# Optimization experiments

Hardware: AMD Instinct MI355X
Metric: run time of the kernel (lower is better)

Reference implementation:

```python
import jax, jax.numpy as jnp
import numpy as np
import math

C = 256
GROUPS = 8  # min(8, C)
EPS = 1e-5


def group_norm(x, gamma, beta):
    # x: [b, c, h, w]
    b, c, h, w = x.shape
    xg = x.reshape(b, GROUPS, c // GROUPS, h, w)
    mean = xg.mean(axis=(2, 3, 4), keepdims=True)
    var = xg.var(axis=(2, 3, 4), keepdims=True)
    xg = (xg - mean) / jnp.sqrt(var + EPS)
    x = xg.reshape(b, c, h, w)
    return x * gamma[None, :, None, None] + beta[None, :, None, None]


def setup_inputs() -> dict:
    key = jax.random.key(0)
    ks = jax.random.split(key, 7)
    b, h, w = 8, 64, 64
    x = jax.random.normal(ks[0], (b, C, h, w), dtype=jnp.float32)
    gn_w = jnp.ones((C,), dtype=jnp.float32)
    gn_b = jnp.zeros((C,), dtype=jnp.float32)
    # 1x1 convs as [out, in] matrices (kaiming-uniform-like scale)
    s = 1.0 / math.sqrt(C)
    qkv_w = jax.random.uniform(ks[1], (3 * C, C), minval=-s, maxval=s, dtype=jnp.float32)
    qkv_b = jax.random.uniform(ks[2], (3 * C,), minval=-s, maxval=s, dtype=jnp.float32)
    out_w = jax.random.uniform(ks[3], (C, C), minval=-s, maxval=s, dtype=jnp.float32)
    out_b = jax.random.uniform(ks[4], (C,), minval=-s, maxval=s, dtype=jnp.float32)
    return {"x": x, "gn_w": gn_w, "gn_b": gn_b, "qkv_w": qkv_w,
            "qkv_b": qkv_b, "out_w": out_w, "out_b": out_b}


def reference(x, gn_w, gn_b, qkv_w, qkv_b, out_w, out_b):
    b, c, h, w = x.shape
    xn = group_norm(x, gn_w, gn_b)  # residual uses normalized x (as in source)
    # 1x1 conv to qkv: [b, 3c, h, w]
    qkv = jnp.einsum('oc,bchw->bohw', qkv_w, xn) + qkv_b[None, :, None, None]
    q, k, v = jnp.split(qkv, 3, axis=1)
    # flatten spatial -> [b, hw, c]
    def flat(t):
        return t.transpose(0, 2, 3, 1).reshape(b, h * w, c)
    q, k, v = flat(q), flat(k), flat(v)
    scores = jnp.einsum('bnc,bmc->bnm', q, k) / math.sqrt(c)  # [b, hw, hw]
    attn = jax.nn.softmax(scores, axis=-1)
    out = jnp.einsum('bnm,bmc->bnc', attn, v)  # [b, hw, c]
    out = out.reshape(b, h, w, c).transpose(0, 3, 1, 2)  # [b, c, h, w]
    out = jnp.einsum('oc,bchw->bohw', out_w, out) + out_b[None, :, None, None]
    return out + xn
```

## Files before the change

kernel.cpp:

```cpp
#include <hip/hip_runtime.h>
#include <hip/hip_bf16.h>

#define BATCH 8
#define CH 256
#define HWSZ 4096
#define NGROUPS 8
#define CPG 32
#define GSIZE (CPG * HWSZ)

typedef unsigned short u16;
typedef short bf16x8 __attribute__((ext_vector_type(8)));
typedef float f32x4 __attribute__((ext_vector_type(4)));
typedef unsigned int u32x4 __attribute__((ext_vector_type(4)));

union Frag8 {
    bf16x8 v;
    u32x4 q;
    u16 s[8];
};

static __device__ inline u16 f2bf(float f) {
    unsigned int u = __float_as_uint(f);
    u = u + 0x7fffu + ((u >> 16) & 1u);
    return (u16)(u >> 16);
}

static __device__ inline unsigned int pk2bf(float a, float b) {
    __hip_bfloat162 h2 = __float22bfloat162_rn(make_float2(a, b));
    unsigned int r;
    __builtin_memcpy(&r, &h2, 4);
    return r;
}

__global__ __launch_bounds__(256) void gn_stats_part_k(const float* __restrict__ x,
                                                       float* __restrict__ partial) {
    int blk = blockIdx.x;
    int bg = blk >> 3, chunk = blk & 7;
    const float4* base = (const float4*)(x + (size_t)bg * GSIZE + (size_t)chunk * (GSIZE / 8));
    float s = 0.f, ss = 0.f;
    for (int i = threadIdx.x; i < GSIZE / 8 / 4; i += 256) {
        float4 v = base[i];
        s += v.x + v.y + v.z + v.w;
        ss += v.x * v.x + v.y * v.y + v.z * v.z + v.w * v.w;
    }
    #pragma unroll
    for (int off = 32; off > 0; off >>= 1) {
        s += __shfl_xor(s, off, 64);
        ss += __shfl_xor(ss, off, 64);
    }
    __shared__ float red[8];
    int wid = threadIdx.x >> 6;
    if ((threadIdx.x & 63) == 0) { red[wid * 2] = s; red[wid * 2 + 1] = ss; }
    __syncthreads();
    if (threadIdx.x == 0) {
        float S = red[0] + red[2] + red[4] + red[6];
        float SS = red[1] + red[3] + red[5] + red[7];
        atomicAdd(&partial[bg * 2], S);
        atomicAdd(&partial[bg * 2 + 1], SS);
    }
}

__global__ void gn_finalize_k(const float* __restrict__ partial, float* __restrict__ stats) {
    int bg = threadIdx.x;
    float S = partial[bg * 2], SS = partial[bg * 2 + 1];
    float mean = S / (float)GSIZE;
    float var = SS / (float)GSIZE - mean * mean;
    stats[bg * 2] = mean;
    stats[bg * 2 + 1] = rsqrtf(var + 1e-5f);
}

#define TPAD 258
__global__ __launch_bounds__(256) void gn_apply_k(const float* __restrict__ x,
                                                  const float* __restrict__ stats,
                                                  const float* __restrict__ gw,
                                                  const float* __restrict__ gb,
                                                  float* __restrict__ xnf,
                                                  u16* __restrict__ xnt) {
    int b = blockIdx.x >> 6;
    int hw0 = (blockIdx.x & 63) * 64;
    __shared__ u16 lds[64 * TPAD];
    __shared__ float sw[CH], sb[CH], smean[NGROUPS], srstd[NGROUPS];
    if (threadIdx.x < CH) { sw[threadIdx.x] = gw[threadIdx.x]; sb[threadIdx.x] = gb[threadIdx.x]; }
    if (threadIdx.x < NGROUPS) {
        smean[threadIdx.x] = stats[(b * NGROUPS + threadIdx.x) * 2];
        srstd[threadIdx.x] = stats[(b * NGROUPS + threadIdx.x) * 2 + 1];
    }
    __syncthreads();
    for (int it = 0; it < 64; ++it) {
        int idx = it * 256 + threadIdx.x;
        int c = idx >> 6, hwl = idx & 63;
        size_t g = ((size_t)b * CH + c) * HWSZ + hw0 + hwl;
        float v = x[g];
        int grp = c >> 5;
        float xn = (v - smean[grp]) * srstd[grp] * sw[c] + sb[c];
        xnf[g] = xn;
        lds[hwl * TPAD + c] = f2bf(xn);
    }
    __syncthreads();
    int hwl = threadIdx.x >> 2, cb = (threadIdx.x & 3) * 64;
    u16* dst = xnt + ((size_t)b * HWSZ + hw0 + hwl) * CH + cb;
    for (int j = 0; j < 64; j += 8) {
        u16 tmp[8];
        #pragma unroll
        for (int k = 0; k < 8; ++k) tmp[k] = lds[hwl * TPAD + cb + j + k];
        *(u32x4*)(dst + j) = *(u32x4*)tmp;
    }
}

__global__ __launch_bounds__(256) void qkv_gemm_k(const float* __restrict__ w,
                                                  const float* __restrict__ bias,
                                                  const u16* __restrict__ xnt,
                                                  u16* __restrict__ qws,
                                                  u16* __restrict__ kws,
                                                  u16* __restrict__ vws) {
    int b = blockIdx.z;
    int o0 = blockIdx.y * 64;
    int n0 = blockIdx.x * 64;
    int w_id = threadIdx.x >> 6;
    int lane = threadIdx.x & 63;
    int jr = lane & 15, g = lane >> 4;
    int orow = o0 + w_id * 16 + jr;
    f32x4 acc[4] = {};
    for (int kk = 0; kk < 8; ++kk) {
        const float* ap = w + (size_t)orow * CH + kk * 32 + g * 8;
        Frag8 af;
        #pragma unroll
        for (int e = 0; e < 8; ++e) af.s[e] = f2bf(ap[e]);
        #pragma unroll
        for (int s = 0; s < 4; ++s) {
            const u16* bp = xnt + ((size_t)b * HWSZ + n0 + s * 16 + jr) * CH + kk * 32 + g * 8;
            Frag8 bfr; bfr.q = *(const u32x4*)bp;
            acc[s] = __builtin_amdgcn_mfma_f32_16x16x32_bf16(af.v, bfr.v, acc[s], 0, 0, 0);
        }
    }
    #pragma unroll
    for (int s = 0; s < 4; ++s) {
        #pragma unroll
        for (int r = 0; r < 4; ++r) {
            int o = o0 + w_id * 16 + g * 4 + r;
            int n = n0 + s * 16 + jr;
            float val = acc[s][r] + bias[o];
            if (o < 256)       qws[((size_t)b * HWSZ + n) * CH + o] = f2bf(val * 0.0625f);
            else if (o < 512)  kws[((size_t)b * HWSZ + n) * CH + (o - 256)] = f2bf(val);
            else               vws[((size_t)b * CH + (o - 512)) * HWSZ + n] = f2bf(val);
        }
    }
}

#define PSTRIDE 72
#define NW 8
__global__ __launch_bounds__(512, 1) void attn_k(const u16* __restrict__ qws,
                                                 const u16* __restrict__ kws,
                                                 const u16* __restrict__ vws,
                                                 u16* __restrict__ ows) {
    __shared__ u16 kbuf[2][64 * 256];
    __shared__ u16 vbuf[2][256 * 64];
    __shared__ u16 plds[NW][16 * PSTRIDE];

    int b = blockIdx.y;
    int q0 = blockIdx.x * 128;
    int tid = threadIdx.x;
    int w_id = tid >> 6;
    int lane = tid & 63;
    int jr = lane & 15, g = lane >> 4;

    const char* kgbase = (const char*)(kws + ((size_t)b * HWSZ) * CH);
    const char* vgbase = (const char*)(vws + ((size_t)b * CH) * HWSZ);

    Frag8 qa[8];
    const u16* qbase = qws + ((size_t)b * HWSZ + q0 + w_id * 16 + jr) * CH;
    #pragma unroll
    for (int kk = 0; kk < 8; ++kk) qa[kk].q = *(const u32x4*)(qbase + kk * 32 + g * 8);

    auto stage = [&](int bufi, int kt) {
        int k0 = kt * 64;
        char* kd = (char*)&kbuf[bufi][0];
        char* vd = (char*)&vbuf[bufi][0];
        #pragma unroll
        for (int ii = 0; ii < 4; ++ii) {
            int i = w_id * 4 + ii;
            int r = i * 2 + (lane >> 5);
            int bl = (lane & 31) * 16;
            int bs = bl ^ ((r & 7) << 4);
            const char* src = kgbase + ((size_t)(k0 + r)) * 512 + bs;
            __builtin_amdgcn_global_load_lds(
                (const __attribute__((address_space(1))) void*)src,
                (__attribute__((address_space(3))) void*)(kd + i * 1024), 16, 0, 0);
        }
        #pragma unroll
        for (int ii = 0; ii < 4; ++ii) {
            int i = w_id * 4 + ii;
            int r = i * 8 + (lane >> 3);
            int bl = (lane & 7) * 16;
            int bs = bl ^ ((r & 7) << 4);
            const char* src = vgbase + (size_t)r * 8192 + (size_t)k0 * 2 + bs;
            __builtin_amdgcn_global_load_lds(
                (const __attribute__((address_space(1))) void*)src,
                (__attribute__((address_space(3))) void*)(vd + i * 1024), 16, 0, 0);
        }
    };

    float m_run = -1e30f, l_run = 0.f;
    f32x4 acc[16] = {};

    stage(0, 0);
    int bufi = 0;

    for (int kt = 0; kt < 64; ++kt) {
        if (kt + 1 < 64) {
            stage(bufi ^ 1, kt + 1);
            asm volatile("s_waitcnt vmcnt(8)" ::: "memory");
        } else {
            asm volatile("s_waitcnt vmcnt(0)" ::: "memory");
        }
        __builtin_amdgcn_s_barrier();

        const char* kb = (const char*)&kbuf[bufi][0];
        const char* vb = (const char*)&vbuf[bufi][0];

        f32x4 sacc[4] = {};
        __builtin_amdgcn_s_setprio(1);
        #pragma unroll
        for (int kk = 0; kk < 8; ++kk) {
            #pragma unroll
            for (int s = 0; s < 4; ++s) {
                int r = s * 16 + jr;
                int cb = kk * 64 + g * 16;
                Frag8 kf; kf.q = *(const u32x4*)(kb + r * 512 + (cb ^ ((r & 7) << 4)));
                sacc[s] = __builtin_amdgcn_mfma_f32_16x16x32_bf16(kf.v, qa[kk].v, sacc[s], 0, 0, 0);
            }
        }
        __builtin_amdgcn_s_setprio(0);

        float mx = sacc[0][0];
        #pragma unroll
        for (int s = 0; s < 4; ++s)
            #pragma unroll
            for (int r = 0; r < 4; ++r) mx = fmaxf(mx, sacc[s][r]);
        mx = fmaxf(mx, __shfl_xor(mx, 16, 64));
        mx = fmaxf(mx, __shfl_xor(mx, 32, 64));

        if (__any(mx > m_run + 8.f)) {
            float mnew = fmaxf(m_run, mx);
            float alpha = __expf(m_run - mnew);
            #pragma unroll
            for (int cs = 0; cs < 16; ++cs)
                #pragma unroll
                for (int r = 0; r < 4; ++r) acc[cs][r] *= alpha;
            l_run *= alpha;
            m_run = mnew;
        }

        float p[4][4];
        float rs = 0.f;
        #pragma unroll
        for (int s = 0; s < 4; ++s)
            #pragma unroll
            for (int r = 0; r < 4; ++r) {
                float pv = __expf(sacc[s][r] - m_run);
                p[s][r] = pv;
                rs += pv;
            }
        rs += __shfl_xor(rs, 16, 64);
        rs += __shfl_xor(rs, 32, 64);
        l_run += rs;

        #pragma unroll
        for (int s = 0; s < 4; ++s)
            #pragma unroll
            for (int i = 0; i < 2; ++i) {
                unsigned int pk = pk2bf(p[s][2 * i], p[s][2 * i + 1]);
                *(unsigned int*)&plds[w_id][jr * PSTRIDE + s * 16 + g * 4 + 2 * i] = pk;
            }

        __builtin_amdgcn_s_setprio(1);
        #pragma unroll
        for (int kk = 0; kk < 2; ++kk) {
            Frag8 pa;
            pa.q = *(const u32x4*)&plds[w_id][jr * PSTRIDE + kk * 32 + g * 8];
            #pragma unroll
            for (int cs = 0; cs < 16; ++cs) {
                int r = cs * 16 + jr;
                int cb = kk * 64 + g * 16;
                Frag8 vf; vf.q = *(const u32x4*)(vb + r * 128 + (cb ^ ((r & 7) << 4)));
                acc[cs] = __builtin_amdgcn_mfma_f32_16x16x32_bf16(vf.v, pa.v, acc[cs], 0, 0, 0);
            }
        }
        __builtin_amdgcn_s_setprio(0);

        asm volatile("s_waitcnt lgkmcnt(0)" ::: "memory");
        __builtin_amdgcn_s_barrier();
        bufi ^= 1;
    }

    float inv_l = 1.0f / l_run;
    int n = q0 + w_id * 16 + jr;
    u16* obase = ows + ((size_t)b * HWSZ + n) * CH;
    #pragma unroll
    for (int cs = 0; cs < 16; ++cs) {
        #pragma unroll
        for (int i = 0; i < 2; ++i) {
            int c = cs * 16 + g * 4 + 2 * i;
            unsigned int pk = pk2bf(acc[cs][2 * i] * inv_l, acc[cs][2 * i + 1] * inv_l);
            *(unsigned int*)&obase[c] = pk;
        }
    }
}

__global__ __launch_bounds__(256) void proj_k(const float* __restrict__ w,
                                              const float* __restrict__ bias,
                                              const u16* __restrict__ ows,
                                              const float* __restrict__ xnf,
                                              float* __restrict__ out) {
    int b = blockIdx.z;
    int o0 = blockIdx.y * 64;
    int n0 = blockIdx.x * 64;
    int w_id = threadIdx.x >> 6;
    int lane = threadIdx.x & 63;
    int jr = lane & 15, g = lane >> 4;
    int orow = o0 + w_id * 16 + jr;
    f32x4 acc[4] = {};
    for (int kk = 0; kk < 8; ++kk) {
        const float* ap = w + (size_t)orow * CH + kk * 32 + g * 8;
        Frag8 af;
        #pragma unroll
        for (int e = 0; e < 8; ++e) af.s[e] = f2bf(ap[e]);
        #pragma unroll
        for (int s = 0; s < 4; ++s) {
            const u16* bp = ows + ((size_t)b * HWSZ + n0 + s * 16 + jr) * CH + kk * 32 + g * 8;
            Frag8 bfr; bfr.q = *(const u32x4*)bp;
            acc[s] = __builtin_amdgcn_mfma_f32_16x16x32_bf16(af.v, bfr.v, acc[s], 0, 0, 0);
        }
    }
    #pragma unroll
    for (int s = 0; s < 4; ++s) {
        #pragma unroll
        for (int r = 0; r < 4; ++r) {
            int o = o0 + w_id * 16 + g * 4 + r;
            int n = n0 + s * 16 + jr;
            size_t gaddr = ((size_t)b * CH + o) * HWSZ + n;
            out[gaddr] = acc[s][r] + bias[o] + xnf[gaddr];
        }
    }
}

extern "C" void kernel_launch(void* const* d_in, const int* in_sizes, int n_in,
                              void* d_out, int out_size, void* d_ws, size_t ws_size,
                              hipStream_t stream) {
    const float* x     = (const float*)d_in[0];
    const float* gn_w  = (const float*)d_in[1];
    const float* gn_b  = (const float*)d_in[2];
    const float* qkv_w = (const float*)d_in[3];
    const float* qkv_b = (const float*)d_in[4];
    const float* out_w = (const float*)d_in[5];
    const float* out_b = (const float*)d_in[6];
    float* out = (float*)d_out;

    char* ws = (char*)d_ws;
    const size_t NB = (size_t)BATCH * HWSZ * CH;
    float* stats   = (float*)ws;
    float* partial = (float*)(ws + 512);
    float* xnf     = (float*)(ws + 1024);
    size_t off = 1024 + NB * 4;
    u16* xnt = (u16*)(ws + off); off += NB * 2;
    u16* qws = (u16*)(ws + off); off += NB * 2;
    u16* kws = (u16*)(ws + off); off += NB * 2;
    u16* vws = (u16*)(ws + off); off += NB * 2;
    u16* ows = (u16*)(ws + off); off += NB * 2;

    hipMemsetAsync(partial, 0, 64 * 2 * sizeof(float), stream);
    gn_stats_part_k<<<dim3(512), dim3(256), 0, stream>>>(x, partial);
    gn_finalize_k<<<dim3(1), dim3(64), 0, stream>>>(partial, stats);
    gn_apply_k<<<dim3(512), dim3(256), 0, stream>>>(x, stats, gn_w, gn_b, xnf, xnt);
    qkv_gemm_k<<<dim3(64, 12, 8), dim3(256), 0, stream>>>(qkv_w, qkv_b, xnt, qws, kws, vws);
    attn_k<<<dim3(32, 8), dim3(512), 0, stream>>>(qws, kws, vws, ows);
    proj_k<<<dim3(64, 4, 8), dim3(256), 0, stream>>>(out_w, out_b, ows, xnf, out);
}
```

Measured before the change: 484.3 us.

## Switch attention to 32x32x16 MFMA with register-resident P and 4 waves

The attention kernel moves from 16x16x32 MFMA tiles to 32x32x16 tiles, with each wave owning 32 query rows and the block shrinking from 8 to 4 waves. The P matrix is now rearranged into B-operand fragments with cross-half lane shuffles instead of a round trip through LDS, so the per-wave P buffer is removed. Larger tiles raise the compute per LDS fragment load of K and V. The cost is higher register pressure from 128 accumulator floats and fewer waves to hide latency, and each wave now issues twice as many staging loads.

```diff
diff --git a/kernel.cpp b/kernel.cpp
--- a/kernel.cpp
+++ b/kernel.cpp
@@ -9,8 +9,10 @@
 #define GSIZE (CPG * HWSZ)
 
 typedef unsigned short u16;
+typedef unsigned int u32;
 typedef short bf16x8 __attribute__((ext_vector_type(8)));
 typedef float f32x4 __attribute__((ext_vector_type(4)));
+typedef float f32x16 __attribute__((ext_vector_type(16)));
 typedef unsigned int u32x4 __attribute__((ext_vector_type(4)));
 
 union Frag8 {
@@ -25,9 +27,9 @@
     return (u16)(u >> 16);
 }
 
-static __device__ inline unsigned int pk2bf(float a, float b) {
+static __device__ inline u32 pk2bf(float a, float b) {
     __hip_bfloat162 h2 = __float22bfloat162_rn(make_float2(a, b));
-    unsigned int r;
+    u32 r;
     __builtin_memcpy(&r, &h2, 4);
     return r;
 }
@@ -147,38 +149,36 @@
     }
 }
 
-#define PSTRIDE 72
-#define NW 8
-__global__ __launch_bounds__(512, 1) void attn_k(const u16* __restrict__ qws,
+__global__ __launch_bounds__(256, 1) void attn_k(const u16* __restrict__ qws,
                                                  const u16* __restrict__ kws,
                                                  const u16* __restrict__ vws,
                                                  u16* __restrict__ ows) {
     __shared__ u16 kbuf[2][64 * 256];
     __shared__ u16 vbuf[2][256 * 64];
-    __shared__ u16 plds[NW][16 * PSTRIDE];
 
     int b = blockIdx.y;
     int q0 = blockIdx.x * 128;
     int tid = threadIdx.x;
     int w_id = tid >> 6;
     int lane = tid & 63;
-    int jr = lane & 15, g = lane >> 4;
+    int qcol = lane & 31;
+    int hi = lane >> 5;
 
     const char* kgbase = (const char*)(kws + ((size_t)b * HWSZ) * CH);
     const char* vgbase = (const char*)(vws + ((size_t)b * CH) * HWSZ);
 
-    Frag8 qa[8];
-    const u16* qbase = qws + ((size_t)b * HWSZ + q0 + w_id * 16 + jr) * CH;
-    #pragma unroll
-    for (int kk = 0; kk < 8; ++kk) qa[kk].q = *(const u32x4*)(qbase + kk * 32 + g * 8);
+    Frag8 qf[16];
+    const u16* qbase = qws + ((size_t)b * HWSZ + q0 + w_id * 32 + qcol) * CH + hi * 8;
+    #pragma unroll
+    for (int ks = 0; ks < 16; ++ks) qf[ks].q = *(const u32x4*)(qbase + ks * 16);
 
     auto stage = [&](int bufi, int kt) {
         int k0 = kt * 64;
         char* kd = (char*)&kbuf[bufi][0];
         char* vd = (char*)&vbuf[bufi][0];
         #pragma unroll
-        for (int ii = 0; ii < 4; ++ii) {
-            int i = w_id * 4 + ii;
+        for (int ii = 0; ii < 8; ++ii) {
+            int i = w_id * 8 + ii;
             int r = i * 2 + (lane >> 5);
             int bl = (lane & 31) * 16;
             int bs = bl ^ ((r & 7) << 4);
@@ -188,8 +188,8 @@
                 (__attribute__((address_space(3))) void*)(kd + i * 1024), 16, 0, 0);
         }
         #pragma unroll
-        for (int ii = 0; ii < 4; ++ii) {
-            int i = w_id * 4 + ii;
+        for (int ii = 0; ii < 8; ++ii) {
+            int i = w_id * 8 + ii;
             int r = i * 8 + (lane >> 3);
             int bl = (lane & 7) * 16;
             int bs = bl ^ ((r & 7) << 4);
@@ -201,7 +201,7 @@
     };
 
     float m_run = -1e30f, l_run = 0.f;
-    f32x4 acc[16] = {};
+    f32x16 acc[8] = {};
 
     stage(0, 0);
     int bufi = 0;
@@ -209,7 +209,7 @@
     for (int kt = 0; kt < 64; ++kt) {
         if (kt + 1 < 64) {
             stage(bufi ^ 1, kt + 1);
-            asm volatile("s_waitcnt vmcnt(8)" ::: "memory");
+            asm volatile("s_waitcnt vmcnt(16)" ::: "memory");
         } else {
             asm volatile("s_waitcnt vmcnt(0)" ::: "memory");
         }
@@ -218,72 +218,89 @@
         const char* kb = (const char*)&kbuf[bufi][0];
         const char* vb = (const char*)&vbuf[bufi][0];
 
-        f32x4 sacc[4] = {};
+        f32x16 sacc[2] = {};
         __builtin_amdgcn_s_setprio(1);
         #pragma unroll
-        for (int kk = 0; kk < 8; ++kk) {
-            #pragma unroll
-            for (int s = 0; s < 4; ++s) {
-                int r = s * 16 + jr;
-                int cb = kk * 64 + g * 16;
+        for (int ks = 0; ks < 16; ++ks) {
+            #pragma unroll
+            for (int t = 0; t < 2; ++t) {
+                int r = t * 32 + qcol;
+                int cb = ks * 32 + hi * 16;
                 Frag8 kf; kf.q = *(const u32x4*)(kb + r * 512 + (cb ^ ((r & 7) << 4)));
-                sacc[s] = __builtin_amdgcn_mfma_f32_16x16x32_bf16(kf.v, qa[kk].v, sacc[s], 0, 0, 0);
+                sacc[t] = __builtin_amdgcn_mfma_f32_32x32x16_bf16(kf.v, qf[ks].v, sacc[t], 0, 0, 0);
             }
         }
         __builtin_amdgcn_s_setprio(0);
 
         float mx = sacc[0][0];
         #pragma unroll
-        for (int s = 0; s < 4; ++s)
-            #pragma unroll
-            for (int r = 0; r < 4; ++r) mx = fmaxf(mx, sacc[s][r]);
-        mx = fmaxf(mx, __shfl_xor(mx, 16, 64));
+        for (int t = 0; t < 2; ++t)
+            #pragma unroll
+            for (int e = 0; e < 16; ++e) mx = fmaxf(mx, sacc[t][e]);
         mx = fmaxf(mx, __shfl_xor(mx, 32, 64));
 
         if (__any(mx > m_run + 8.f)) {
             float mnew = fmaxf(m_run, mx);
             float alpha = __expf(m_run - mnew);
             #pragma unroll
-            for (int cs = 0; cs < 16; ++cs)
+            for (int dt = 0; dt < 8; ++dt)
                 #pragma unroll
-                for (int r = 0; r < 4; ++r) acc[cs][r] *= alpha;
+                for (int e = 0; e < 16; ++e) acc[dt][e] *= alpha;
             l_run *= alpha;
             m_run = mnew;
         }
 
-        float p[4][4];
+        float p_[2][16];
         float rs = 0.f;
         #pragma unroll
-        for (int s = 0; s < 4; ++s)
-            #pragma unroll
-            for (int r = 0; r < 4; ++r) {
-                float pv = __expf(sacc[s][r] - m_run);
-                p[s][r] = pv;
+        for (int t = 0; t < 2; ++t)
+            #pragma unroll
+            for (int e = 0; e < 16; ++e) {
+                float pv = __expf(sacc[t][e] - m_run);
+                p_[t][e] = pv;
                 rs += pv;
             }
-        rs += __shfl_xor(rs, 16, 64);
         rs += __shfl_xor(rs, 32, 64);
         l_run += rs;
 
-        #pragma unroll
-        for (int s = 0; s < 4; ++s)
-            #pragma unroll
-            for (int i = 0; i < 2; ++i) {
-                unsigned int pk = pk2bf(p[s][2 * i], p[s][2 * i + 1]);
-                *(unsigned int*)&plds[w_id][jr * PSTRIDE + s * 16 + g * 4 + 2 * i] = pk;
+        u32 pk_[2][4][2];
+        #pragma unroll
+        for (int t = 0; t < 2; ++t)
+            #pragma unroll
+            for (int d = 0; d < 4; ++d) {
+                pk_[t][d][0] = pk2bf(p_[t][4 * d + 0], p_[t][4 * d + 1]);
+                pk_[t][d][1] = pk2bf(p_[t][4 * d + 2], p_[t][4 * d + 3]);
             }
 
+        Frag8 pf[4];
+        #pragma unroll
+        for (int kstep = 0; kstep < 4; ++kstep) {
+            const int j0 = 2 * kstep, j1 = 2 * kstep + 1;
+            u32 x0a = pk_[j0 >> 2][j0 & 3][0], x0b = pk_[j0 >> 2][j0 & 3][1];
+            u32 x1a = pk_[j1 >> 2][j1 & 3][0], x1b = pk_[j1 >> 2][j1 & 3][1];
+            u32 s0 = hi ? x0a : x1a;
+            u32 s1 = hi ? x0b : x1b;
+            u32 r0 = __shfl_xor(s0, 32, 64);
+            u32 r1 = __shfl_xor(s1, 32, 64);
+            u32 a0 = hi ? x1a : x0a;
+            u32 a1 = hi ? x1b : x0b;
+            u32x4 f;
+            f[0] = hi ? r0 : a0;
+            f[1] = hi ? r1 : a1;
+            f[2] = hi ? a0 : r0;
+            f[3] = hi ? a1 : r1;
+            pf[kstep].q = f;
+        }
+
         __builtin_amdgcn_s_setprio(1);
         #pragma unroll
-        for (int kk = 0; kk < 2; ++kk) {
-            Frag8 pa;
-            pa.q = *(const u32x4*)&plds[w_id][jr * PSTRIDE + kk * 32 + g * 8];
-            #pragma unroll
-            for (int cs = 0; cs < 16; ++cs) {
-                int r = cs * 16 + jr;
-                int cb = kk * 64 + g * 16;
-                Frag8 vf; vf.q = *(const u32x4*)(vb + r * 128 + (cb ^ ((r & 7) << 4)));
-                acc[cs] = __builtin_amdgcn_mfma_f32_16x16x32_bf16(vf.v, pa.v, acc[cs], 0, 0, 0);
+        for (int dt = 0; dt < 8; ++dt) {
+            #pragma unroll
+            for (int kstep = 0; kstep < 4; ++kstep) {
+                int rr = dt * 32 + qcol;
+                int cb = kstep * 32 + hi * 16;
+                Frag8 vf; vf.q = *(const u32x4*)(vb + rr * 128 + (cb ^ ((rr & 7) << 4)));
+                acc[dt] = __builtin_amdgcn_mfma_f32_32x32x16_bf16(vf.v, pf[kstep].v, acc[dt], 0, 0, 0);
             }
         }
         __builtin_amdgcn_s_setprio(0);
@@ -294,15 +311,17 @@
     }
 
     float inv_l = 1.0f / l_run;
-    int n = q0 + w_id * 16 + jr;
+    int n = q0 + w_id * 32 + qcol;
     u16* obase = ows + ((size_t)b * HWSZ + n) * CH;
     #pragma unroll
-    for (int cs = 0; cs < 16; ++cs) {
-        #pragma unroll
-        for (int i = 0; i < 2; ++i) {
-            int c = cs * 16 + g * 4 + 2 * i;
-            unsigned int pk = pk2bf(acc[cs][2 * i] * inv_l, acc[cs][2 * i + 1] * inv_l);
-            *(unsigned int*)&obase[c] = pk;
+    for (int dt = 0; dt < 8; ++dt) {
+        #pragma unroll
+        for (int rq = 0; rq < 4; ++rq) {
+            int cbase = dt * 32 + 8 * rq + 4 * hi;
+            u32 w0 = pk2bf(acc[dt][4 * rq + 0] * inv_l, acc[dt][4 * rq + 1] * inv_l);
+            u32 w1 = pk2bf(acc[dt][4 * rq + 2] * inv_l, acc[dt][4 * rq + 3] * inv_l);
+            *(u32*)&obase[cbase] = w0;
+            *(u32*)&obase[cbase + 2] = w1;
         }
     }
 }
@@ -373,6 +392,6 @@
     gn_finalize_k<<<dim3(1), dim3(64), 0, stream>>>(partial, stats);
     gn_apply_k<<<dim3(512), dim3(256), 0, stream>>>(x, stats, gn_w, gn_b, xnf, xnt);
     qkv_gemm_k<<<dim3(64, 12, 8), dim3(256), 0, stream>>>(qkv_w, qkv_b, xnt, qws, kws, vws);
-    attn_k<<<dim3(32, 8), dim3(512), 0, stream>>>(qws, kws, vws, ows);
+    attn_k<<<dim3(32, 8), dim3(256), 0, stream>>>(qws, kws, vws, ows);
     proj_k<<<dim3(64, 4, 8), dim3(256), 0, stream>>>(out_w, out_b, ows, xnf, out);
 }
```

Measured after the change: 511.5 us. +5.6%, slower.
